# Kernel optimization log

Measured on AMD Instinct MI355X. Metric: run time of the kernel, lower is better.

The kernel has to match this reference:

```python
import jax, jax.numpy as jnp
import numpy as np

N_NODES = 100000
N_EDGES = 1600000
D_FEAT = 128
HIDDEN = 100
N_CLASSES = 10


def gcn_conv(x, edge_index, W, b):
    """PyG GCNConv: add self-loops, symmetric deg^-1/2 normalization,
    linear transform, gather-scale-scatter aggregation, bias."""
    n = x.shape[0]
    loop = jnp.arange(n, dtype=edge_index.dtype)
    src = jnp.concatenate([edge_index[0], loop])  # message sources
    dst = jnp.concatenate([edge_index[1], loop])  # message targets
    # degree of target nodes (edge weight = 1), including self-loops
    deg = jax.ops.segment_sum(jnp.ones_like(dst, dtype=x.dtype), dst, num_segments=n)
    dinv = jnp.where(deg > 0, deg ** -0.5, 0.0).astype(x.dtype)
    norm = dinv[src] * dinv[dst]  # [E+N]
    h = x @ W  # [N, out]
    msg = h[src] * norm[:, None]  # gather + normalize
    out = jax.ops.segment_sum(msg, dst, num_segments=n)  # scatter-add
    return out + b


def setup_inputs() -> dict:
    key = jax.random.key(0)
    k1, k2, k3, k4 = jax.random.split(key, 4)
    x = jax.random.normal(k1, (N_NODES, D_FEAT), dtype=jnp.float32)
    edge_index = jax.random.randint(k2, (2, N_EDGES), 0, N_NODES, dtype=jnp.int64)
    W1 = jax.random.normal(k3, (D_FEAT, HIDDEN), dtype=jnp.float32) * (1.0 / np.sqrt(D_FEAT))
    b1 = jnp.zeros((HIDDEN,), dtype=jnp.float32)
    W2 = jax.random.normal(k4, (HIDDEN, N_CLASSES), dtype=jnp.float32) * (1.0 / np.sqrt(HIDDEN))
    b2 = jnp.zeros((N_CLASSES,), dtype=jnp.float32)
    return {"x": x, "edge_index": edge_index, "W1": W1, "b1": b1, "W2": W2, "b2": b2}


def reference(x, edge_index, W1, b1, W2, b2):
    h = gcn_conv(x, edge_index, W1, b1)
    h = jax.nn.relu(h)
    # F.dropout(training=self.training): inference mode -> identity
    h = gcn_conv(h, edge_index, W2, b2)
    # global_mean_pool with batch = zeros -> mean over all nodes, keep batch dim
    pooled = jnp.mean(h, axis=0, keepdims=True)  # [1, n_classes]
    return jax.nn.log_softmax(pooled, axis=1)
```

## Files before the change

### kernel.cpp

```cpp
#include <hip/hip_runtime.h>
#include <hip/hip_bf16.h>
#include <math.h>

#define N_NODES 100000
#define N_EDGES 1600000
#define D_FEAT 128
#define HIDDEN 100
#define N_CLASSES 10

#define NB 391
#define ACAP 5120
#define PTILE 8192
#define NPBLK ((N_EDGES + PTILE - 1) / PTILE)

#define OFF_BCURD  0
#define OFF_BCURS  6256
#define OFF_BBASE  12512
#define OFF_SPART  12912
#define OFF_CSUM   38512
#define OFF_DINV   138512
#define OFF_ROWPTR 238512
#define OFF_CSRC   338516
#define OFF_ARENAD 1938516
#define OFF_ARENAS 3940436
#define OFF_H1Q    5942356
#define OFF_WF     7542356

#define LAMBDA 0.125f

typedef __attribute__((ext_vector_type(8))) short bf16x8;
typedef __attribute__((ext_vector_type(4))) float f32x4;

__device__ inline unsigned pack_bf16x2(float a, float b) {
    unsigned ua = __float_as_uint(a); ua = (ua + 0x7FFFu + ((ua >> 16) & 1u)) >> 16;
    unsigned ub = __float_as_uint(b); ub = (ub + 0x7FFFu + ((ub >> 16) & 1u)) >> 16;
    return ua | (ub << 16);
}

__device__ inline unsigned short bf16_1(float a) {
    unsigned ua = __float_as_uint(a);
    return (unsigned short)((ua + 0x7FFFu + ((ua >> 16) & 1u)) >> 16);
}

__device__ inline unsigned enc_i4(float v, float s8) {
    float a = fmaf(v, s8, 8.0f);
    a = fminf(fmaxf(a, 0.0f), 15.0f);
    return (unsigned)(int)rintf(a);
}

__global__ void k_init(int* __restrict__ bcurD, int* __restrict__ bcurS,
                       float* __restrict__ S_part) {
    int i = blockIdx.x * blockDim.x + threadIdx.x;
    if (i < 256 * 100) S_part[i] = 0.0f;
    if (i < NB) { bcurD[i * 16] = i * ACAP; bcurS[i * 16] = i * ACAP; }
}

__global__ __launch_bounds__(256) void k_part2(const int* __restrict__ src,
                                               const int* __restrict__ dst,
                                               int* __restrict__ bcurD,
                                               int* __restrict__ bcurS,
                                               unsigned* __restrict__ arenaD,
                                               unsigned* __restrict__ arenaS) {
    __shared__ int histD[NB], histS[NB];
    __shared__ int gbD[NB], gbS[NB];
    __shared__ int curD[NB], curS[NB];
    int t = threadIdx.x;
    int e0 = blockIdx.x * PTILE;
    int n = N_EDGES - e0; if (n > PTILE) n = PTILE;

    for (int i = t; i < NB; i += 256) { histD[i] = 0; histS[i] = 0; }
    __syncthreads();
    for (int i = t; i < n; i += 256) {
        atomicAdd(&histD[dst[e0 + i] >> 8], 1);
        atomicAdd(&histS[src[e0 + i] >> 8], 1);
    }
    __syncthreads();
    for (int b = t; b < NB; b += 256) {
        int cD = histD[b]; gbD[b] = cD ? atomicAdd(&bcurD[b * 16], cD) : 0; curD[b] = 0;
        int cS = histS[b]; gbS[b] = cS ? atomicAdd(&bcurS[b * 16], cS) : 0; curS[b] = 0;
    }
    __syncthreads();
    for (int i = t; i < n; i += 256) {
        int s = src[e0 + i];
        int d = dst[e0 + i];
        int bD = d >> 8;
        int pD = atomicAdd(&curD[bD], 1);
        arenaD[(unsigned)(gbD[bD] + pD)] = (unsigned)s | ((unsigned)(d & 255) << 20);
        int bS = s >> 8;
        int pS = atomicAdd(&curS[bS], 1);
        arenaS[(unsigned)(gbS[bS] + pS)] = (unsigned)d | ((unsigned)(s & 255) << 20);
    }
}

__global__ void k_scan391(const int* __restrict__ bcurD, int* __restrict__ bbase,
                          int* __restrict__ rowptr) {
    __shared__ int sh[512];
    int t = threadIdx.x;
    int c = (t < NB) ? (bcurD[t * 16] - t * ACAP) : 0;
    sh[t] = c;
    __syncthreads();
    for (int off = 1; off < 512; off <<= 1) {
        int a = (t >= off) ? sh[t - off] : 0;
        __syncthreads();
        sh[t] += a;
        __syncthreads();
    }
    if (t < NB) bbase[t] = sh[t] - c;
    if (t == NB - 1) rowptr[N_NODES] = sh[t];
}

__global__ __launch_bounds__(256) void k_fillB(const unsigned* __restrict__ arenaD,
                                               const int* __restrict__ bcurD,
                                               const int* __restrict__ bbase,
                                               float* __restrict__ dinv,
                                               int* __restrict__ rowptr,
                                               int* __restrict__ csr_src) {
    __shared__ int hist[256];
    __shared__ int sh[256];
    __shared__ int cur[256];
    int b = blockIdx.x;
    int t = threadIdx.x;
    int v0 = b << 8;
    int nv = N_NODES - v0; if (nv > 256) nv = 256;
    int cnt = bcurD[b * 16] - b * ACAP;
    const unsigned* A = arenaD + (size_t)b * ACAP;

    hist[t] = 0;
    __syncthreads();
    for (int i = t; i < cnt; i += 256) atomicAdd(&hist[A[i] >> 20], 1);
    __syncthreads();
    int h = hist[t];
    if (t < nv) dinv[v0 + t] = rsqrtf((float)(h + 1));
    sh[t] = h;
    __syncthreads();
    for (int off = 1; off < 256; off <<= 1) {
        int a = (t >= off) ? sh[t - off] : 0;
        __syncthreads();
        sh[t] += a;
        __syncthreads();
    }
    int excl = sh[t] - h;
    int base = bbase[b];
    if (t < nv) rowptr[v0 + t] = base + excl;
    cur[t] = excl;
    __syncthreads();
    for (int i = t; i < cnt; i += 256) {
        unsigned p = A[i];
        int pos = atomicAdd(&cur[p >> 20], 1);
        csr_src[base + pos] = (int)(p & 0xFFFFFu);
    }
}

__global__ __launch_bounds__(256) void k_csumB(const unsigned* __restrict__ arenaS,
                                               const int* __restrict__ bcurS,
                                               const float* __restrict__ dinv,
                                               float* __restrict__ csum) {
    __shared__ float cs[256];
    int b = blockIdx.x, t = threadIdx.x;
    int cnt = bcurS[b * 16] - b * ACAP;
    const unsigned* A = arenaS + (size_t)b * ACAP;
    cs[t] = 0.0f;
    __syncthreads();
    for (int i = t; i < cnt; i += 256) {
        unsigned p = A[i];
        atomicAdd(&cs[p >> 20], dinv[p & 0xFFFFFu]);
    }
    __syncthreads();
    int v = (b << 8) + t;
    if (v < N_NODES) csum[v] = cs[t];
}

__global__ void k_prepW(const float* __restrict__ W1, unsigned short* __restrict__ Wf) {
    int i = blockIdx.x * 256 + threadIdx.x;
    int nt = i >> 8, rem = i & 255;
    int ks = rem >> 6, lane = rem & 63;
    int c = nt * 16 + (lane & 15);
    int k0 = ks * 32 + ((lane >> 4) << 3);
    unsigned short v[8];
#pragma unroll
    for (int j = 0; j < 8; ++j) {
        float f = (c < HIDDEN) ? W1[(k0 + j) * HIDDEN + c] : 0.0f;
        v[j] = bf16_1(f);
    }
    unsigned short* p = Wf + (size_t)((ks * 7 + nt) * 64 + lane) * 8;
#pragma unroll
    for (int j = 0; j < 8; ++j) p[j] = v[j];
}

__global__ __launch_bounds__(256) void k_gemm_mfma(const float* __restrict__ x,
                                                   const unsigned short* __restrict__ Wf,
                                                   const float* __restrict__ dinv,
                                                   unsigned* __restrict__ h1q) {
    __shared__ unsigned short As[64][136];
    __shared__ unsigned char Cs[64][112];
    int t = threadIdx.x;
    long long r0 = (long long)blockIdx.x * 64;

    const float4* xv = (const float4*)(x + r0 * D_FEAT);
    for (int i = t; i < 2048; i += 256) {
        int r = i >> 5, q = i & 31;
        float4 v;
        if (r0 + r < N_NODES) v = xv[i];
        else { v.x = v.y = v.z = v.w = 0.0f; }
        uint2 pv;
        pv.x = pack_bf16x2(v.x, v.y);
        pv.y = pack_bf16x2(v.z, v.w);
        *(uint2*)&As[r][q * 4] = pv;
    }
    __syncthreads();

    int wave = t >> 6, lane = t & 63;
    int rbase = wave * 16;
    int arow = rbase + (lane & 15);
    int kgrp = lane >> 4;

    f32x4 acc[7];
#pragma unroll
    for (int nt = 0; nt < 7; ++nt) acc[nt] = (f32x4){0.0f, 0.0f, 0.0f, 0.0f};

    const bf16x8* Bf = (const bf16x8*)Wf;
#pragma unroll
    for (int ks = 0; ks < 4; ++ks) {
        bf16x8 a = *(const bf16x8*)&As[arow][ks * 32 + kgrp * 8];
#pragma unroll
        for (int nt = 0; nt < 7; ++nt) {
            bf16x8 b = Bf[(ks * 7 + nt) * 64 + lane];
            acc[nt] = __builtin_amdgcn_mfma_f32_16x16x32_bf16(a, b, acc[nt], 0, 0, 0);
        }
    }

    float s8[4];
#pragma unroll
    for (int i = 0; i < 4; ++i) {
        long long idx = r0 + rbase + kgrp * 4 + i;
        s8[i] = (idx < N_NODES) ? 8.0f * dinv[idx] : 0.0f;
    }
    int ccol = lane & 15;
#pragma unroll
    for (int nt = 0; nt < 7; ++nt) {
#pragma unroll
        for (int i = 0; i < 4; ++i) {
            unsigned code = enc_i4(acc[nt][i], s8[i]);
            Cs[rbase + kgrp * 4 + i][nt * 16 + ccol] = (unsigned char)code;
        }
    }
    __syncthreads();

    for (int i = t; i < 1024; i += 256) {
        int r = i >> 4, w = i & 15;
        unsigned wq = 0;
        if (w < 14) {
            const unsigned* cp = (const unsigned*)&Cs[r][8 * w];
            unsigned c0 = cp[0], c1 = cp[1];
            unsigned t0 = c0 | (c0 >> 4);
            unsigned lo = (t0 & 0xFFu) | ((t0 >> 8) & 0xFF00u);
            unsigned t1 = c1 | (c1 >> 4);
            unsigned hi = (t1 & 0xFFu) | ((t1 >> 8) & 0xFF00u);
            wq = lo | (hi << 16);
        }
        if (r0 + r < N_NODES) h1q[(size_t)(r0 + r) * 16 + w] = wq;
    }
}

#define NPW 4
__global__ __launch_bounds__(256) void k_gather_i4(const int* __restrict__ rowptr,
                                                   const int* __restrict__ csr_src,
                                                   const float* __restrict__ dinv,
                                                   const float* __restrict__ csum,
                                                   const unsigned* __restrict__ h1q,
                                                   const float* __restrict__ b1,
                                                   float* __restrict__ S_part) {
    __shared__ float Sl[HIDDEN];
    int t = threadIdx.x;
    if (t < HIDDEN) Sl[t] = 0.0f;
    __syncthreads();
    int wave = t >> 6, lane = t & 63;
    int u16 = lane & 15, slot = lane >> 4;
    int fbase = u16 * 8;
    float bb[8];
#pragma unroll
    for (int i = 0; i < 8; ++i) bb[i] = (fbase + i < HIDDEN) ? b1[fbase + i] : 0.0f;
    float sacc[8];
#pragma unroll
    for (int i = 0; i < 8; ++i) sacc[i] = 0.0f;
    int vbase = (blockIdx.x * 4 + wave) * NPW;
#pragma unroll 1
    for (int nn = 0; nn < NPW; ++nn) {
        int v = vbase + nn;
        float dv = dinv[v];
        int jb = rowptr[v], je = rowptr[v + 1];
        unsigned ws = (slot == 0) ? h1q[(size_t)v * 16 + u16] : 0u;
        unsigned accE = ws & 0x0F0F0F0Fu;
        unsigned accO = (ws >> 4) & 0x0F0F0F0Fu;
#pragma unroll 1
        for (int j = jb; j < je; j += 8) {
            int j0 = j + slot, j1 = j + 4 + slot;
            unsigned w0 = (j0 < je) ? h1q[(size_t)csr_src[j0] * 16 + u16] : 0u;
            unsigned w1 = (j1 < je) ? h1q[(size_t)csr_src[j1] * 16 + u16] : 0u;
            accE += w0 & 0x0F0F0F0Fu;
            accO += (w0 >> 4) & 0x0F0F0F0Fu;
            accE += w1 & 0x0F0F0F0Fu;
            accO += (w1 >> 4) & 0x0F0F0F0Fu;
        }
        int eL = (int)(accE & 0x00FF00FFu);
        int eH = (int)((accE >> 8) & 0x00FF00FFu);
        int oL = (int)(accO & 0x00FF00FFu);
        int oH = (int)((accO >> 8) & 0x00FF00FFu);
        eL += __shfl_xor(eL, 16, 64); eL += __shfl_xor(eL, 32, 64);
        eH += __shfl_xor(eH, 16, 64); eH += __shfl_xor(eH, 32, 64);
        oL += __shfl_xor(oL, 16, 64); oL += __shfl_xor(oL, 32, 64);
        oH += __shfl_xor(oH, 16, 64); oH += __shfl_xor(oH, 32, 64);
        if (slot == 0) {
            float zc = -8.0f * (float)(je - jb + 1);
            float tv = dv * LAMBDA;
            float cv = dv * (csum[v] + dv);
            int n[8] = { eL & 0xFFFF, oL & 0xFFFF, eH & 0xFFFF, oH & 0xFFFF,
                         eL >> 16,    oL >> 16,    eH >> 16,    oH >> 16 };
#pragma unroll
            for (int i = 0; i < 8; ++i) {
                float z = fmaf(tv, (float)n[i] + zc, bb[i]);
                sacc[i] = fmaf(cv, fmaxf(z, 0.0f), sacc[i]);
            }
        }
    }
    if (slot == 0) {
#pragma unroll
        for (int i = 0; i < 8; ++i) {
            int f = fbase + i;
            if (f < HIDDEN) atomicAdd(&Sl[f], sacc[i]);
        }
    }
    __syncthreads();
    if (t < HIDDEN) atomicAdd(&S_part[(blockIdx.x & 255) * 100 + t], Sl[t]);
}

__global__ void k_final(const float* __restrict__ S_part, const float* __restrict__ W2,
                        const float* __restrict__ b2, float* __restrict__ out) {
    __shared__ float Sl[HIDDEN];
    __shared__ float p[16];
    int t = threadIdx.x;
    if (t < HIDDEN) {
        float s = 0.0f;
        for (int r = 0; r < 256; ++r) s += S_part[r * 100 + t];
        Sl[t] = s;
    }
    __syncthreads();
    if (t < N_CLASSES) {
        float s = 0.0f;
        for (int f = 0; f < HIDDEN; ++f) s += Sl[f] * W2[f * N_CLASSES + t];
        p[t] = s * (1.0f / (float)N_NODES) + b2[t];
    }
    __syncthreads();
    if (t == 0) {
        float m = -INFINITY;
        for (int i = 0; i < N_CLASSES; ++i) m = fmaxf(m, p[i]);
        float se = 0.0f;
        for (int i = 0; i < N_CLASSES; ++i) se += expf(p[i] - m);
        float ls = logf(se);
        for (int i = 0; i < N_CLASSES; ++i) out[i] = p[i] - m - ls;
    }
}

extern "C" void kernel_launch(void* const* d_in, const int* in_sizes, int n_in,
                              void* d_out, int out_size, void* d_ws, size_t ws_size,
                              hipStream_t stream) {
    const float* x  = (const float*)d_in[0];
    const int*   ei = (const int*)d_in[1];
    const float* W1 = (const float*)d_in[2];
    const float* b1 = (const float*)d_in[3];
    const float* W2 = (const float*)d_in[4];
    const float* b2 = (const float*)d_in[5];
    float* out = (float*)d_out;

    const int* src = ei;
    const int* dst = ei + N_EDGES;

    int*            wsi     = (int*)d_ws;
    float*          wsf     = (float*)d_ws;
    int*            bcurD   = wsi + OFF_BCURD;
    int*            bcurS   = wsi + OFF_BCURS;
    int*            bbase   = wsi + OFF_BBASE;
    float*          S_part  = wsf + OFF_SPART;
    float*          csum    = wsf + OFF_CSUM;
    float*          dinv    = wsf + OFF_DINV;
    int*            rowptr  = wsi + OFF_ROWPTR;
    int*            csr_src = wsi + OFF_CSRC;
    unsigned*       arenaD  = (unsigned*)(wsi + OFF_ARENAD);
    unsigned*       arenaS  = (unsigned*)(wsi + OFF_ARENAS);
    unsigned*       h1q     = (unsigned*)(wsi + OFF_H1Q);
    unsigned short* Wf      = (unsigned short*)(wsi + OFF_WF);

    const int nodeBlocks = (N_NODES + 255) / 256;

    k_init<<<nodeBlocks, 256, 0, stream>>>(bcurD, bcurS, S_part);
    k_part2<<<NPBLK, 256, 0, stream>>>(src, dst, bcurD, bcurS, arenaD, arenaS);
    k_scan391<<<1, 512, 0, stream>>>(bcurD, bbase, rowptr);
    k_fillB<<<NB, 256, 0, stream>>>(arenaD, bcurD, bbase, dinv, rowptr, csr_src);
    k_csumB<<<NB, 256, 0, stream>>>(arenaS, bcurS, dinv, csum);

    k_prepW<<<7, 256, 0, stream>>>(W1, Wf);
    k_gemm_mfma<<<(N_NODES + 63) / 64, 256, 0, stream>>>(x, Wf, dinv, h1q);

    k_gather_i4<<<N_NODES / (4 * NPW), 256, 0, stream>>>(rowptr, csr_src, dinv, csum,
                                                         h1q, b1, S_part);
    k_final<<<1, 128, 0, stream>>>(S_part, W2, b2, out);
}
```

Before: 189.8 us.

## Replace CSR build and gather with bucketed shared-memory scatter aggregation

Drops the full CSR construction (scan kernel, fill kernel, rowptr and csr_src) and instead aggregates layer-1 messages straight from the destination-bucketed arena. Each block handles 128 nodes and accumulates packed int4 features with shared-memory atomics. Bucket granularity shrinks from 256 to 128 nodes, and the per-block partial sums are written directly, which removes the S_part zeroing and the global atomics. This saves two kernels and a CSR write and read pass, at the cost of heavy LDS atomic traffic and more blocks reduced in the final kernel.

Result: slower. 218.5 us (+15.1%).

```diff
diff --git a/kernel.cpp b/kernel.cpp
--- a/kernel.cpp
+++ b/kernel.cpp
@@ -8,23 +8,22 @@
 #define HIDDEN 100
 #define N_CLASSES 10
 
-#define NB 391
-#define ACAP 5120
+#define BSHIFT 7
+#define NBK 782
+#define ACAP 2816
 #define PTILE 8192
 #define NPBLK ((N_EDGES + PTILE - 1) / PTILE)
 
 #define OFF_BCURD  0
-#define OFF_BCURS  6256
-#define OFF_BBASE  12512
-#define OFF_SPART  12912
-#define OFF_CSUM   38512
-#define OFF_DINV   138512
-#define OFF_ROWPTR 238512
-#define OFF_CSRC   338516
-#define OFF_ARENAD 1938516
-#define OFF_ARENAS 3940436
-#define OFF_H1Q    5942356
-#define OFF_WF     7542356
+#define OFF_BCURS  12512
+#define OFF_SPART  25024
+#define OFF_CSUM   103224
+#define OFF_DINV   203224
+#define OFF_DEG    303224
+#define OFF_ARENAD 353224
+#define OFF_ARENAS 2555336
+#define OFF_H1Q    4757448
+#define OFF_WF     6357448
 
 #define LAMBDA 0.125f
 
@@ -48,11 +47,9 @@
     return (unsigned)(int)rintf(a);
 }
 
-__global__ void k_init(int* __restrict__ bcurD, int* __restrict__ bcurS,
-                       float* __restrict__ S_part) {
+__global__ void k_init(int* __restrict__ bcurD, int* __restrict__ bcurS) {
     int i = blockIdx.x * blockDim.x + threadIdx.x;
-    if (i < 256 * 100) S_part[i] = 0.0f;
-    if (i < NB) { bcurD[i * 16] = i * ACAP; bcurS[i * 16] = i * ACAP; }
+    if (i < NBK) { bcurD[i * 16] = i * ACAP; bcurS[i * 16] = i * ACAP; }
 }
 
 __global__ __launch_bounds__(256) void k_part2(const int* __restrict__ src,
@@ -61,21 +58,21 @@
                                                int* __restrict__ bcurS,
                                                unsigned* __restrict__ arenaD,
                                                unsigned* __restrict__ arenaS) {
-    __shared__ int histD[NB], histS[NB];
-    __shared__ int gbD[NB], gbS[NB];
-    __shared__ int curD[NB], curS[NB];
+    __shared__ int histD[NBK], histS[NBK];
+    __shared__ int gbD[NBK], gbS[NBK];
+    __shared__ int curD[NBK], curS[NBK];
     int t = threadIdx.x;
     int e0 = blockIdx.x * PTILE;
     int n = N_EDGES - e0; if (n > PTILE) n = PTILE;
 
-    for (int i = t; i < NB; i += 256) { histD[i] = 0; histS[i] = 0; }
+    for (int i = t; i < NBK; i += 256) { histD[i] = 0; histS[i] = 0; }
     __syncthreads();
     for (int i = t; i < n; i += 256) {
-        atomicAdd(&histD[dst[e0 + i] >> 8], 1);
-        atomicAdd(&histS[src[e0 + i] >> 8], 1);
-    }
-    __syncthreads();
-    for (int b = t; b < NB; b += 256) {
+        atomicAdd(&histD[dst[e0 + i] >> BSHIFT], 1);
+        atomicAdd(&histS[src[e0 + i] >> BSHIFT], 1);
+    }
+    __syncthreads();
+    for (int b = t; b < NBK; b += 256) {
         int cD = histD[b]; gbD[b] = cD ? atomicAdd(&bcurD[b * 16], cD) : 0; curD[b] = 0;
         int cS = histS[b]; gbS[b] = cS ? atomicAdd(&bcurS[b * 16], cS) : 0; curS[b] = 0;
     }
@@ -83,71 +80,33 @@
     for (int i = t; i < n; i += 256) {
         int s = src[e0 + i];
         int d = dst[e0 + i];
-        int bD = d >> 8;
+        int bD = d >> BSHIFT;
         int pD = atomicAdd(&curD[bD], 1);
-        arenaD[(unsigned)(gbD[bD] + pD)] = (unsigned)s | ((unsigned)(d & 255) << 20);
-        int bS = s >> 8;
+        arenaD[(unsigned)(gbD[bD] + pD)] = (unsigned)s | ((unsigned)(d & 127) << 20);
+        int bS = s >> BSHIFT;
         int pS = atomicAdd(&curS[bS], 1);
-        arenaS[(unsigned)(gbS[bS] + pS)] = (unsigned)d | ((unsigned)(s & 255) << 20);
-    }
-}
-
-__global__ void k_scan391(const int* __restrict__ bcurD, int* __restrict__ bbase,
-                          int* __restrict__ rowptr) {
-    __shared__ int sh[512];
-    int t = threadIdx.x;
-    int c = (t < NB) ? (bcurD[t * 16] - t * ACAP) : 0;
-    sh[t] = c;
-    __syncthreads();
-    for (int off = 1; off < 512; off <<= 1) {
-        int a = (t >= off) ? sh[t - off] : 0;
-        __syncthreads();
-        sh[t] += a;
-        __syncthreads();
-    }
-    if (t < NB) bbase[t] = sh[t] - c;
-    if (t == NB - 1) rowptr[N_NODES] = sh[t];
-}
-
-__global__ __launch_bounds__(256) void k_fillB(const unsigned* __restrict__ arenaD,
-                                               const int* __restrict__ bcurD,
-                                               const int* __restrict__ bbase,
-                                               float* __restrict__ dinv,
-                                               int* __restrict__ rowptr,
-                                               int* __restrict__ csr_src) {
-    __shared__ int hist[256];
-    __shared__ int sh[256];
-    __shared__ int cur[256];
-    int b = blockIdx.x;
-    int t = threadIdx.x;
-    int v0 = b << 8;
-    int nv = N_NODES - v0; if (nv > 256) nv = 256;
+        arenaS[(unsigned)(gbS[bS] + pS)] = (unsigned)d | ((unsigned)(s & 127) << 20);
+    }
+}
+
+__global__ __launch_bounds__(256) void k_degB(const unsigned* __restrict__ arenaD,
+                                              const int* __restrict__ bcurD,
+                                              float* __restrict__ dinv,
+                                              unsigned short* __restrict__ deg) {
+    __shared__ int hist[128];
+    int b = blockIdx.x, t = threadIdx.x;
+    int v0 = b << BSHIFT;
+    int nv = N_NODES - v0; if (nv > 128) nv = 128;
     int cnt = bcurD[b * 16] - b * ACAP;
     const unsigned* A = arenaD + (size_t)b * ACAP;
-
-    hist[t] = 0;
+    if (t < 128) hist[t] = 0;
     __syncthreads();
     for (int i = t; i < cnt; i += 256) atomicAdd(&hist[A[i] >> 20], 1);
     __syncthreads();
-    int h = hist[t];
-    if (t < nv) dinv[v0 + t] = rsqrtf((float)(h + 1));
-    sh[t] = h;
-    __syncthreads();
-    for (int off = 1; off < 256; off <<= 1) {
-        int a = (t >= off) ? sh[t - off] : 0;
-        __syncthreads();
-        sh[t] += a;
-        __syncthreads();
-    }
-    int excl = sh[t] - h;
-    int base = bbase[b];
-    if (t < nv) rowptr[v0 + t] = base + excl;
-    cur[t] = excl;
-    __syncthreads();
-    for (int i = t; i < cnt; i += 256) {
-        unsigned p = A[i];
-        int pos = atomicAdd(&cur[p >> 20], 1);
-        csr_src[base + pos] = (int)(p & 0xFFFFFu);
+    if (t < nv) {
+        int h = hist[t];
+        deg[v0 + t] = (unsigned short)h;
+        dinv[v0 + t] = rsqrtf((float)(h + 1));
     }
 }
 
@@ -155,19 +114,20 @@
                                                const int* __restrict__ bcurS,
                                                const float* __restrict__ dinv,
                                                float* __restrict__ csum) {
-    __shared__ float cs[256];
+    __shared__ float cs[128];
     int b = blockIdx.x, t = threadIdx.x;
+    int v0 = b << BSHIFT;
+    int nv = N_NODES - v0; if (nv > 128) nv = 128;
     int cnt = bcurS[b * 16] - b * ACAP;
     const unsigned* A = arenaS + (size_t)b * ACAP;
-    cs[t] = 0.0f;
+    if (t < 128) cs[t] = 0.0f;
     __syncthreads();
     for (int i = t; i < cnt; i += 256) {
         unsigned p = A[i];
         atomicAdd(&cs[p >> 20], dinv[p & 0xFFFFFu]);
     }
     __syncthreads();
-    int v = (b << 8) + t;
-    if (v < N_NODES) csum[v] = cs[t];
+    if (t < nv) csum[v0 + t] = cs[t];
 }
 
 __global__ void k_prepW(const float* __restrict__ W1, unsigned short* __restrict__ Wf) {
@@ -262,92 +222,119 @@
     }
 }
 
-#define NPW 4
-__global__ __launch_bounds__(256) void k_gather_i4(const int* __restrict__ rowptr,
-                                                   const int* __restrict__ csr_src,
-                                                   const float* __restrict__ dinv,
-                                                   const float* __restrict__ csum,
-                                                   const unsigned* __restrict__ h1q,
-                                                   const float* __restrict__ b1,
-                                                   float* __restrict__ S_part) {
-    __shared__ float Sl[HIDDEN];
-    int t = threadIdx.x;
-    if (t < HIDDEN) Sl[t] = 0.0f;
-    __syncthreads();
-    int wave = t >> 6, lane = t & 63;
+__global__ __launch_bounds__(256) void k_aggB(const unsigned* __restrict__ arenaD,
+                                              const int* __restrict__ bcurD,
+                                              const unsigned* __restrict__ h1q,
+                                              const float* __restrict__ dinv,
+                                              const float* __restrict__ csum,
+                                              const unsigned short* __restrict__ deg,
+                                              const float* __restrict__ b1,
+                                              float* __restrict__ S_part) {
+    __shared__ unsigned acc[128 * 52];
+    __shared__ float tvL[128], cvL[128], wzL[128];
+    __shared__ float SlH[2][HIDDEN];
+    int b = blockIdx.x, t = threadIdx.x;
+    int v0 = b << BSHIFT;
+    int nv = N_NODES - v0; if (nv > 128) nv = 128;
+
+    for (int i = t; i < 128 * 52; i += 256) acc[i] = 0u;
+    if (t < 128) {
+        float dv = 0.0f, cs_ = 0.0f; int dg = 0;
+        if (t < nv) {
+            dv = dinv[v0 + t];
+            cs_ = csum[v0 + t];
+            dg = (int)deg[v0 + t];
+        }
+        float tv = dv * LAMBDA;
+        tvL[t] = tv;
+        cvL[t] = dv * (cs_ + dv);
+        wzL[t] = -tv * 8.0f * (float)(dg + 1);
+    }
+    __syncthreads();
+
+    int lane = t & 63, wave = t >> 6;
     int u16 = lane & 15, slot = lane >> 4;
-    int fbase = u16 * 8;
-    float bb[8];
-#pragma unroll
-    for (int i = 0; i < 8; ++i) bb[i] = (fbase + i < HIDDEN) ? b1[fbase + i] : 0.0f;
-    float sacc[8];
-#pragma unroll
-    for (int i = 0; i < 8; ++i) sacc[i] = 0.0f;
-    int vbase = (blockIdx.x * 4 + wave) * NPW;
-#pragma unroll 1
-    for (int nn = 0; nn < NPW; ++nn) {
-        int v = vbase + nn;
-        float dv = dinv[v];
-        int jb = rowptr[v], je = rowptr[v + 1];
-        unsigned ws = (slot == 0) ? h1q[(size_t)v * 16 + u16] : 0u;
-        unsigned accE = ws & 0x0F0F0F0Fu;
-        unsigned accO = (ws >> 4) & 0x0F0F0F0Fu;
-#pragma unroll 1
-        for (int j = jb; j < je; j += 8) {
-            int j0 = j + slot, j1 = j + 4 + slot;
-            unsigned w0 = (j0 < je) ? h1q[(size_t)csr_src[j0] * 16 + u16] : 0u;
-            unsigned w1 = (j1 < je) ? h1q[(size_t)csr_src[j1] * 16 + u16] : 0u;
-            accE += w0 & 0x0F0F0F0Fu;
-            accO += (w0 >> 4) & 0x0F0F0F0Fu;
-            accE += w1 & 0x0F0F0F0Fu;
-            accO += (w1 >> 4) & 0x0F0F0F0Fu;
-        }
-        int eL = (int)(accE & 0x00FF00FFu);
-        int eH = (int)((accE >> 8) & 0x00FF00FFu);
-        int oL = (int)(accO & 0x00FF00FFu);
-        int oH = (int)((accO >> 8) & 0x00FF00FFu);
-        eL += __shfl_xor(eL, 16, 64); eL += __shfl_xor(eL, 32, 64);
-        eH += __shfl_xor(eH, 16, 64); eH += __shfl_xor(eH, 32, 64);
-        oL += __shfl_xor(oL, 16, 64); oL += __shfl_xor(oL, 32, 64);
-        oH += __shfl_xor(oH, 16, 64); oH += __shfl_xor(oH, 32, 64);
-        if (slot == 0) {
-            float zc = -8.0f * (float)(je - jb + 1);
-            float tv = dv * LAMBDA;
-            float cv = dv * (csum[v] + dv);
-            int n[8] = { eL & 0xFFFF, oL & 0xFFFF, eH & 0xFFFF, oH & 0xFFFF,
-                         eL >> 16,    oL >> 16,    eH >> 16,    oH >> 16 };
-#pragma unroll
-            for (int i = 0; i < 8; ++i) {
-                float z = fmaf(tv, (float)n[i] + zc, bb[i]);
-                sacc[i] = fmaf(cv, fmaxf(z, 0.0f), sacc[i]);
+    int eoff = wave * 4 + slot;
+    int cnt = bcurD[b * 16] - b * ACAP;
+    const unsigned* A = arenaD + (size_t)b * ACAP;
+
+    for (int e0 = 0; e0 < cnt; e0 += 32) {
+        int eA = e0 + eoff, eB = e0 + 16 + eoff;
+        unsigned pA = 0xFFFFFFFFu, pB = 0xFFFFFFFFu;
+        if (eA < cnt) pA = A[eA];
+        if (eB < cnt) pB = A[eB];
+        unsigned wA = 0u, wB = 0u;
+        if (pA != 0xFFFFFFFFu) wA = h1q[(size_t)(pA & 0xFFFFFu) * 16 + u16];
+        if (pB != 0xFFFFFFFFu) wB = h1q[(size_t)(pB & 0xFFFFFu) * 16 + u16];
+        if (u16 < 13) {
+            if (pA != 0xFFFFFFFFu) {
+                unsigned* base = &acc[(int)(pA >> 20) * 52 + u16 * 4];
+                unsigned ev = wA & 0x0F0F0F0Fu, od = (wA >> 4) & 0x0F0F0F0Fu;
+                atomicAdd(base + 0, (ev & 0xFu) | ((od & 0xFu) << 16));
+                atomicAdd(base + 1, ((ev >> 8) & 0xFu) | (((od >> 8) & 0xFu) << 16));
+                atomicAdd(base + 2, ((ev >> 16) & 0xFu) | (((od >> 16) & 0xFu) << 16));
+                atomicAdd(base + 3, ((ev >> 24) & 0xFu) | ((od >> 24) << 16));
             }
-        }
-    }
-    if (slot == 0) {
-#pragma unroll
-        for (int i = 0; i < 8; ++i) {
-            int f = fbase + i;
-            if (f < HIDDEN) atomicAdd(&Sl[f], sacc[i]);
-        }
-    }
-    __syncthreads();
-    if (t < HIDDEN) atomicAdd(&S_part[(blockIdx.x & 255) * 100 + t], Sl[t]);
+            if (pB != 0xFFFFFFFFu) {
+                unsigned* base = &acc[(int)(pB >> 20) * 52 + u16 * 4];
+                unsigned ev = wB & 0x0F0F0F0Fu, od = (wB >> 4) & 0x0F0F0F0Fu;
+                atomicAdd(base + 0, (ev & 0xFu) | ((od & 0xFu) << 16));
+                atomicAdd(base + 1, ((ev >> 8) & 0xFu) | (((od >> 8) & 0xFu) << 16));
+                atomicAdd(base + 2, ((ev >> 16) & 0xFu) | (((od >> 16) & 0xFu) << 16));
+                atomicAdd(base + 3, ((ev >> 24) & 0xFu) | ((od >> 24) << 16));
+            }
+        }
+    }
+    for (int i = t; i < nv * 16; i += 256) {
+        int r = i >> 4, u = i & 15;
+        unsigned w = h1q[(size_t)(v0 + r) * 16 + u];
+        if (u < 13) {
+            unsigned* base = &acc[r * 52 + u * 4];
+            unsigned ev = w & 0x0F0F0F0Fu, od = (w >> 4) & 0x0F0F0F0Fu;
+            atomicAdd(base + 0, (ev & 0xFu) | ((od & 0xFu) << 16));
+            atomicAdd(base + 1, ((ev >> 8) & 0xFu) | (((od >> 8) & 0xFu) << 16));
+            atomicAdd(base + 2, ((ev >> 16) & 0xFu) | (((od >> 16) & 0xFu) << 16));
+            atomicAdd(base + 3, ((ev >> 24) & 0xFu) | ((od >> 24) << 16));
+        }
+    }
+    __syncthreads();
+
+    if (t < 200) {
+        int half = (t >= 100) ? 1 : 0;
+        int f = t - half * 100;
+        int p = f >> 1, sh = (f & 1) << 4;
+        float bf = b1[f];
+        float sacc = 0.0f;
+        int n0 = half * 64, n1 = n0 + 64; if (n1 > nv) n1 = nv;
+        for (int n = n0; n < n1; ++n) {
+            unsigned val = acc[n * 52 + p];
+            float nf = (float)((val >> sh) & 0xFFFFu);
+            float z = fmaf(tvL[n], nf, wzL[n] + bf);
+            sacc = fmaf(cvL[n], fmaxf(z, 0.0f), sacc);
+        }
+        SlH[half][f] = sacc;
+    }
+    __syncthreads();
+    if (t < HIDDEN) S_part[(size_t)b * 100 + t] = SlH[0][t] + SlH[1][t];
 }
 
 __global__ void k_final(const float* __restrict__ S_part, const float* __restrict__ W2,
                         const float* __restrict__ b2, float* __restrict__ out) {
-    __shared__ float Sl[HIDDEN];
+    __shared__ float Sl[4][HIDDEN];
     __shared__ float p[16];
     int t = threadIdx.x;
-    if (t < HIDDEN) {
+    if (t < 400) {
+        int q = t / 100, f = t - q * 100;
         float s = 0.0f;
-        for (int r = 0; r < 256; ++r) s += S_part[r * 100 + t];
-        Sl[t] = s;
-    }
+        for (int r = q; r < NBK; r += 4) s += S_part[(size_t)r * 100 + f];
+        Sl[q][f] = s;
+    }
+    __syncthreads();
+    if (t < HIDDEN) Sl[0][t] = Sl[0][t] + Sl[1][t] + Sl[2][t] + Sl[3][t];
     __syncthreads();
     if (t < N_CLASSES) {
         float s = 0.0f;
-        for (int f = 0; f < HIDDEN; ++f) s += Sl[f] * W2[f * N_CLASSES + t];
+        for (int f = 0; f < HIDDEN; ++f) s += Sl[0][f] * W2[f * N_CLASSES + t];
         p[t] = s * (1.0f / (float)N_NODES) + b2[t];
     }
     __syncthreads();
@@ -375,33 +362,27 @@
     const int* src = ei;
     const int* dst = ei + N_EDGES;
 
-    int*            wsi     = (int*)d_ws;
-    float*          wsf     = (float*)d_ws;
-    int*            bcurD   = wsi + OFF_BCURD;
-    int*            bcurS   = wsi + OFF_BCURS;
-    int*            bbase   = wsi + OFF_BBASE;
-    float*          S_part  = wsf + OFF_SPART;
-    float*          csum    = wsf + OFF_CSUM;
-    float*          dinv    = wsf + OFF_DINV;
-    int*            rowptr  = wsi + OFF_ROWPTR;
-    int*            csr_src = wsi + OFF_CSRC;
-    unsigned*       arenaD  = (unsigned*)(wsi + OFF_ARENAD);
-    unsigned*       arenaS  = (unsigned*)(wsi + OFF_ARENAS);
-    unsigned*       h1q     = (unsigned*)(wsi + OFF_H1Q);
-    unsigned short* Wf      = (unsigned short*)(wsi + OFF_WF);
-
-    const int nodeBlocks = (N_NODES + 255) / 256;
-
-    k_init<<<nodeBlocks, 256, 0, stream>>>(bcurD, bcurS, S_part);
+    int*            wsi    = (int*)d_ws;
+    float*          wsf    = (float*)d_ws;
+    int*            bcurD  = wsi + OFF_BCURD;
+    int*            bcurS  = wsi + OFF_BCURS;
+    float*          S_part = wsf + OFF_SPART;
+    float*          csum   = wsf + OFF_CSUM;
+    float*          dinv   = wsf + OFF_DINV;
+    unsigned short* deg    = (unsigned short*)(wsi + OFF_DEG);
+    unsigned*       arenaD = (unsigned*)(wsi + OFF_ARENAD);
+    unsigned*       arenaS = (unsigned*)(wsi + OFF_ARENAS);
+    unsigned*       h1q    = (unsigned*)(wsi + OFF_H1Q);
+    unsigned short* Wf     = (unsigned short*)(wsi + OFF_WF);
+
+    k_init<<<(NBK + 255) / 256, 256, 0, stream>>>(bcurD, bcurS);
     k_part2<<<NPBLK, 256, 0, stream>>>(src, dst, bcurD, bcurS, arenaD, arenaS);
-    k_scan391<<<1, 512, 0, stream>>>(bcurD, bbase, rowptr);
-    k_fillB<<<NB, 256, 0, stream>>>(arenaD, bcurD, bbase, dinv, rowptr, csr_src);
-    k_csumB<<<NB, 256, 0, stream>>>(arenaS, bcurS, dinv, csum);
+    k_degB<<<NBK, 256, 0, stream>>>(arenaD, bcurD, dinv, deg);
+    k_csumB<<<NBK, 256, 0, stream>>>(arenaS, bcurS, dinv, csum);
 
     k_prepW<<<7, 256, 0, stream>>>(W1, Wf);
     k_gemm_mfma<<<(N_NODES + 63) / 64, 256, 0, stream>>>(x, Wf, dinv, h1q);
 
-    k_gather_i4<<<N_NODES / (4 * NPW), 256, 0, stream>>>(rowptr, csr_src, dinv, csum,
-                                                         h1q, b1, S_part);
-    k_final<<<1, 128, 0, stream>>>(S_part, W2, b2, out);
-}
+    k_aggB<<<NBK, 256, 0, stream>>>(arenaD, bcurD, h1q, dinv, csum, deg, b1, S_part);
+    k_final<<<1, 512, 0, stream>>>(S_part, W2, b2, out);
+}
```

## Split quantized hidden table into two feature halves gathered in separate passes

Applied to the files above, without the earlier changes.

The GEMM now writes the int4-packed hidden features into two separate tables, one for features 0-63 and one for 64-127. The gather kernel is launched twice, once per half, with 8 lanes per row and 8 edge slots per wave. Each pass's random-access table is half the size, so it should stay resident in L2 during the gather. The edge loop also uses clamped branchless indices and nontemporal loads for csr_src. The cost is reading the CSR index array twice and one extra kernel launch.

Result: slower. 218.6 us (+15.1%).

```diff
diff --git a/kernel.cpp b/kernel.cpp
--- a/kernel.cpp
+++ b/kernel.cpp
@@ -23,7 +23,8 @@
 #define OFF_CSRC   338516
 #define OFF_ARENAD 1938516
 #define OFF_ARENAS 3940436
-#define OFF_H1Q    5942356
+#define OFF_H1A    5942356
+#define OFF_H1B    6742356
 #define OFF_WF     7542356
 
 #define LAMBDA 0.125f
@@ -190,7 +191,8 @@
 __global__ __launch_bounds__(256) void k_gemm_mfma(const float* __restrict__ x,
                                                    const unsigned short* __restrict__ Wf,
                                                    const float* __restrict__ dinv,
-                                                   unsigned* __restrict__ h1q) {
+                                                   unsigned* __restrict__ h1A,
+                                                   unsigned* __restrict__ h1B) {
     __shared__ unsigned short As[64][136];
     __shared__ unsigned char Cs[64][112];
     int t = threadIdx.x;
@@ -258,16 +260,20 @@
             unsigned hi = (t1 & 0xFFu) | ((t1 >> 8) & 0xFF00u);
             wq = lo | (hi << 16);
         }
-        if (r0 + r < N_NODES) h1q[(size_t)(r0 + r) * 16 + w] = wq;
-    }
-}
-
-#define NPW 4
+        if (r0 + r < N_NODES) {
+            if (w < 8) h1A[(size_t)(r0 + r) * 8 + w] = wq;
+            else       h1B[(size_t)(r0 + r) * 8 + (w - 8)] = wq;
+        }
+    }
+}
+
+#define NPW 2
 __global__ __launch_bounds__(256) void k_gather_i4(const int* __restrict__ rowptr,
                                                    const int* __restrict__ csr_src,
                                                    const float* __restrict__ dinv,
                                                    const float* __restrict__ csum,
-                                                   const unsigned* __restrict__ h1q,
+                                                   const unsigned* __restrict__ tbl,
+                                                   int foff,
                                                    const float* __restrict__ b1,
                                                    float* __restrict__ S_part) {
     __shared__ float Sl[HIDDEN];
@@ -275,8 +281,8 @@
     if (t < HIDDEN) Sl[t] = 0.0f;
     __syncthreads();
     int wave = t >> 6, lane = t & 63;
-    int u16 = lane & 15, slot = lane >> 4;
-    int fbase = u16 * 8;
+    int u8 = lane & 7, slot = lane >> 3;
+    int fbase = foff + u8 * 8;
     float bb[8];
 #pragma unroll
     for (int i = 0; i < 8; ++i) bb[i] = (fbase + i < HIDDEN) ? b1[fbase + i] : 0.0f;
@@ -289,14 +295,21 @@
         int v = vbase + nn;
         float dv = dinv[v];
         int jb = rowptr[v], je = rowptr[v + 1];
-        unsigned ws = (slot == 0) ? h1q[(size_t)v * 16 + u16] : 0u;
+        unsigned ws = (slot == 0) ? tbl[(size_t)v * 8 + u8] : 0u;
         unsigned accE = ws & 0x0F0F0F0Fu;
         unsigned accO = (ws >> 4) & 0x0F0F0F0Fu;
 #pragma unroll 1
-        for (int j = jb; j < je; j += 8) {
-            int j0 = j + slot, j1 = j + 4 + slot;
-            unsigned w0 = (j0 < je) ? h1q[(size_t)csr_src[j0] * 16 + u16] : 0u;
-            unsigned w1 = (j1 < je) ? h1q[(size_t)csr_src[j1] * 16 + u16] : 0u;
+        for (int j = jb; j < je; j += 16) {
+            int j0 = j + slot, j1 = j + 8 + slot;
+            int je1 = je - 1;
+            int c0 = (j0 < je) ? j0 : je1;
+            int c1 = (j1 < je) ? j1 : je1;
+            int s0 = __builtin_nontemporal_load(&csr_src[c0]);
+            int s1 = __builtin_nontemporal_load(&csr_src[c1]);
+            unsigned w0 = tbl[(size_t)s0 * 8 + u8];
+            unsigned w1 = tbl[(size_t)s1 * 8 + u8];
+            w0 = (j0 < je) ? w0 : 0u;
+            w1 = (j1 < je) ? w1 : 0u;
             accE += w0 & 0x0F0F0F0Fu;
             accO += (w0 >> 4) & 0x0F0F0F0Fu;
             accE += w1 & 0x0F0F0F0Fu;
@@ -306,10 +319,10 @@
         int eH = (int)((accE >> 8) & 0x00FF00FFu);
         int oL = (int)(accO & 0x00FF00FFu);
         int oH = (int)((accO >> 8) & 0x00FF00FFu);
-        eL += __shfl_xor(eL, 16, 64); eL += __shfl_xor(eL, 32, 64);
-        eH += __shfl_xor(eH, 16, 64); eH += __shfl_xor(eH, 32, 64);
-        oL += __shfl_xor(oL, 16, 64); oL += __shfl_xor(oL, 32, 64);
-        oH += __shfl_xor(oH, 16, 64); oH += __shfl_xor(oH, 32, 64);
+        eL += __shfl_xor(eL, 8, 64); eL += __shfl_xor(eL, 16, 64); eL += __shfl_xor(eL, 32, 64);
+        eH += __shfl_xor(eH, 8, 64); eH += __shfl_xor(eH, 16, 64); eH += __shfl_xor(eH, 32, 64);
+        oL += __shfl_xor(oL, 8, 64); oL += __shfl_xor(oL, 16, 64); oL += __shfl_xor(oL, 32, 64);
+        oH += __shfl_xor(oH, 8, 64); oH += __shfl_xor(oH, 16, 64); oH += __shfl_xor(oH, 32, 64);
         if (slot == 0) {
             float zc = -8.0f * (float)(je - jb + 1);
             float tv = dv * LAMBDA;
@@ -387,7 +400,8 @@
     int*            csr_src = wsi + OFF_CSRC;
     unsigned*       arenaD  = (unsigned*)(wsi + OFF_ARENAD);
     unsigned*       arenaS  = (unsigned*)(wsi + OFF_ARENAS);
-    unsigned*       h1q     = (unsigned*)(wsi + OFF_H1Q);
+    unsigned*       h1A     = (unsigned*)(wsi + OFF_H1A);
+    unsigned*       h1B     = (unsigned*)(wsi + OFF_H1B);
     unsigned short* Wf      = (unsigned short*)(wsi + OFF_WF);
 
     const int nodeBlocks = (N_NODES + 255) / 256;
@@ -399,9 +413,11 @@
     k_csumB<<<NB, 256, 0, stream>>>(arenaS, bcurS, dinv, csum);
 
     k_prepW<<<7, 256, 0, stream>>>(W1, Wf);
-    k_gemm_mfma<<<(N_NODES + 63) / 64, 256, 0, stream>>>(x, Wf, dinv, h1q);
+    k_gemm_mfma<<<(N_NODES + 63) / 64, 256, 0, stream>>>(x, Wf, dinv, h1A, h1B);
 
     k_gather_i4<<<N_NODES / (4 * NPW), 256, 0, stream>>>(rowptr, csr_src, dinv, csum,
-                                                         h1q, b1, S_part);
+                                                         h1A, 0, b1, S_part);
+    k_gather_i4<<<N_NODES / (4 * NPW), 256, 0, stream>>>(rowptr, csr_src, dinv, csum,
+                                                         h1B, 64, b1, S_part);
     k_final<<<1, 128, 0, stream>>>(S_part, W2, b2, out);
 }
```
